# Kernel optimization log

Hardware: AMD Instinct MI355X
Metric: run time of the kernel (lower is better)

## Reference

```python
import jax, jax.numpy as jnp
import numpy as np
from jax import lax

RATE = 2
KSIZE = 3
STRIDE = 1
FUSE_K = 3
SCALE = 10.0
DN = ('NCHW', 'OIHW', 'NCHW')


def extract_patches(x, k, s):
    # x: [B,C,H,W] -> [B,nH,nW,C,k,k]  (ZeroPad2d(1) when k != 1, as in torch code)
    B, C, H, W = x.shape
    p = 0 if k == 1 else 1
    xp = jnp.pad(x, ((0, 0), (0, 0), (p, p), (p, p)))
    nH = (H + 2 * p - k) // s + 1
    nW = (W + 2 * p - k) // s + 1
    cols = [xp[:, :, di:di + s * nH:s, dj:dj + s * nW:s]
            for di in range(k) for dj in range(k)]
    pat = jnp.stack(cols, 0).reshape(k, k, B, C, nH, nW)
    return pat.transpose(2, 4, 5, 3, 0, 1)


def _fuse(y):
    # conv of the [L,L] score image with eye(FUSE_K) kernel, same padding
    # == sum of diagonal shifts of the zero-padded image
    L = y.shape[0]
    p = (FUSE_K - 1) // 2
    A = jnp.pad(y, ((p, p), (p, p)))
    out = A[0:L, 0:L]
    for d in range(1, FUSE_K):
        out = out + A[d:d + L, d:d + L]
    return out


def _per_sample(xi, wi, raw_wi, mmi, h, w):
    # xi: [C,h,w]  wi: [L,C,3,3]  raw_wi: [L,C,4,4]  mmi: [L,1,1]
    L = h * w
    norm = jnp.sqrt(jnp.sum(wi * wi, axis=(1, 2, 3), keepdims=True))
    wi_n = wi / jnp.maximum(norm, 1e-4)
    # cosine-similarity conv: [L,h,w]
    yi = lax.conv_general_dilated(xi[None], wi_n, (1, 1), ((1, 1), (1, 1)),
                                  dimension_numbers=DN)[0]
    # fuse pass 1 on [L(patch), L(spatial)]
    y = _fuse(yi.reshape(L, L))
    # transpose (h_p,w_p,h',w') -> (w_p,h_p,w',h'), fuse pass 2, transpose back
    y = y.reshape(h, w, h, w).transpose(1, 0, 3, 2).reshape(L, L)
    y = _fuse(y)
    y = y.reshape(w, h, w, h).transpose(1, 0, 3, 2).reshape(L, h, w)
    y = y * mmi
    y = jax.nn.softmax(y * SCALE, axis=0)
    y = jnp.maximum(y * mmi, 1e-8)
    # conv_transpose2d(y, raw_wi, stride=2, padding=1) as lhs-dilated conv
    Wf = raw_wi[:, :, ::-1, ::-1].transpose(1, 0, 2, 3)  # [C,L,4,4]
    out = lax.conv_general_dilated(y[None], Wf, (1, 1), ((2, 2), (2, 2)),
                                   lhs_dilation=(2, 2),
                                   dimension_numbers=DN)[0]
    return out / 4.0


def reference(x1, x2, mask):
    B, C, H, W = x1.shape
    kernel = 2 * RATE
    raw_w = extract_patches(x1, kernel, RATE * STRIDE)
    x2s = x2[:, :, ::2, ::2]          # F.interpolate scale=0.5, nearest
    h, w = x2s.shape[2], x2s.shape[3]
    L = h * w
    raw_w = raw_w.reshape(B, L, C, kernel, kernel)
    wpat = extract_patches(x2s, KSIZE, STRIDE).reshape(B, L, C, KSIZE, KSIZE)
    # mask is already [B,1,h,w]: bilinear align_corners resize to (h,w) is identity
    m = extract_patches(mask, KSIZE, STRIDE).reshape(B, L, -1).mean(axis=2)
    mm = (m == 0.0).astype(x1.dtype)[:, :, None, None]  # [B,L,1,1]
    f = lambda xi, wi, rwi, mmi: _per_sample(xi, wi, rwi, mmi, h, w)
    return jax.vmap(f)(x2s, wpat, raw_w, mm)  # [B,C,H,W]


def setup_inputs() -> dict:
    key = jax.random.key(0)
    k1, k2 = jax.random.split(key)
    x1 = jax.random.normal(k1, (2, 128, 96, 96), dtype=jnp.float32)
    x2 = jax.random.normal(k2, (2, 128, 96, 96), dtype=jnp.float32)
    mask = jnp.zeros((2, 1, 48, 48), dtype=jnp.float32)
    return {"x1": x1, "x2": x2, "mask": mask}
```

## Files before the change

kernel.cpp:

```cpp
#include <hip/hip_runtime.h>
#include <hip/hip_bf16.h>

#define Cc   128
#define Hh   96
#define hs   48
#define Ls   2304
#define CK   2048
#define KG   384

typedef __attribute__((ext_vector_type(8))) short short8;
typedef __attribute__((ext_vector_type(4))) float f32x4;

__device__ __forceinline__ unsigned short f2bf(float x) {
    unsigned int u = __float_as_uint(x);
    unsigned int r = (u + 0x7fff + ((u >> 16) & 1)) >> 16;
    return (unsigned short)r;
}
__device__ __forceinline__ float bf2f(unsigned short h) {
    return __uint_as_float((unsigned)h << 16);
}

__device__ __forceinline__ f32x4 ld4u(const float* p) {
    f32x4 v; __builtin_memcpy(&v, p, 16); return v;
}

#define GLOAD_LDS16(g, l) \
    __builtin_amdgcn_global_load_lds((__attribute__((address_space(1))) const void*)(g), \
                                     (__attribute__((address_space(3))) void*)(l), 16, 0, 0)


__global__ __launch_bounds__(256) void transposePQ_k(const float* __restrict__ x2,
                                                     unsigned short* __restrict__ P,
                                                     unsigned short* __restrict__ Q,
                                                     long long sPQ, int z0) {
    const int z = z0 + blockIdx.z;
    const float* x2b = x2 + (size_t)z * Cc * Hh * Hh;
    unsigned short* Pb = P + (size_t)blockIdx.z * sPQ;
    unsigned short* Qb = Q + (size_t)blockIdx.z * sPQ;
    __shared__ float tile[64][65];
    const int c0 = blockIdx.x * 64;
    const int l0 = blockIdx.y * 64;
    const int t = threadIdx.x;
    const int lt = t & 63, cg = t >> 6;
    const int l = l0 + lt;
    const int iy = l / hs, jx = l % hs;
    const int srcoff = iy * (2 * Hh) + 2 * jx;
#pragma unroll
    for (int cc = 0; cc < 16; ++cc) {
        int c = cg * 16 + cc;
        tile[lt][c] = x2b[(size_t)(c0 + c) * (Hh * Hh) + srcoff];
    }
    __syncthreads();
    const int lr = t >> 2, seg = t & 3;
    const int lw = l0 + lr;
    short8 hv0, hv1, lv0, lv1;
#pragma unroll
    for (int k = 0; k < 8; ++k) {
        float x = tile[lr][seg * 16 + k];
        unsigned short h = f2bf(x);
        float hf = __uint_as_float((unsigned)h << 16);
        unsigned short lo = f2bf(x - hf);
        hv0[k] = (short)h; lv0[k] = (short)lo;
    }
#pragma unroll
    for (int k = 0; k < 8; ++k) {
        float x = tile[lr][seg * 16 + 8 + k];
        unsigned short h = f2bf(x);
        float hf = __uint_as_float((unsigned)h << 16);
        unsigned short lo = f2bf(x - hf);
        hv1[k] = (short)h; lv1[k] = (short)lo;
    }
    size_t rowp = (size_t)lw * KG;
    int coff = c0 + seg * 16;
    *(short8*)&Pb[rowp + coff] = hv0;        *(short8*)&Pb[rowp + coff + 8] = hv1;
    *(short8*)&Pb[rowp + 128 + coff] = lv0;  *(short8*)&Pb[rowp + 128 + coff + 8] = lv1;
    *(short8*)&Pb[rowp + 256 + coff] = hv0;  *(short8*)&Pb[rowp + 256 + coff + 8] = hv1;
    *(short8*)&Qb[rowp + coff] = hv0;        *(short8*)&Qb[rowp + coff + 8] = hv1;
    *(short8*)&Qb[rowp + 128 + coff] = hv0;  *(short8*)&Qb[rowp + 128 + coff + 8] = hv1;
    *(short8*)&Qb[rowp + 256 + coff] = lv0;  *(short8*)&Qb[rowp + 256 + coff + 8] = lv1;
}

__global__ __launch_bounds__(256) void mm_k(const float* __restrict__ mask, float* __restrict__ MM) {
    int z = blockIdx.y;
    const float* mb = mask + (size_t)z * hs * hs;
    float* MMb = MM + (size_t)z * Ls;
    int l = blockIdx.x * 256 + threadIdx.x;
    if (l >= Ls) return;
    int ly = l / hs, lx = l % hs;
    float s = 0.f;
    for (int dy = -1; dy <= 1; ++dy)
        for (int dx = -1; dx <= 1; ++dx) {
            int yy = ly + dy, xx = lx + dx;
            if ((unsigned)yy < (unsigned)hs && (unsigned)xx < (unsigned)hs) s += mb[yy * hs + xx];
        }
    float m = s * (1.0f / 9.0f);
    MMb[l] = (m == 0.0f) ? 1.0f : 0.0f;
}

__global__ __launch_bounds__(256) void taps9rn_k(const float* __restrict__ G, float* __restrict__ S,
                                                 float* __restrict__ RN, long long zsG, long long zsS, int z0) {
    const float* Gb = G + (size_t)blockIdx.z * zsG;
    float* Sb = S + (size_t)blockIdx.z * zsS;
    float* RNb = RN + (size_t)(z0 + blockIdx.z) * Ls;
    int g = blockIdx.x * 256 + threadIdx.x;
    int i = g / 576;
    int jb = (g - i * 576) * 4;
    int iy = i / hs, ix = i % hs;
    int jy = jb / hs, jx0 = jb % hs;
    f32x4 acc = {};
#pragma unroll
    for (int dy = -1; dy <= 1; ++dy) {
        int vy = ((unsigned)(iy + dy) < (unsigned)hs) && ((unsigned)(jy + dy) < (unsigned)hs);
#pragma unroll
        for (int dx = -1; dx <= 1; ++dx) {
            int vi = vy && ((unsigned)(ix + dx) < (unsigned)hs);
            int o = hs * dy + dx;
            int row = vi ? (i + o) : i;
            f32x4 v = ld4u(&Gb[(size_t)row * Ls + jb + o]);
            f32x4 m;
#pragma unroll
            for (int ln = 0; ln < 4; ++ln)
                m[ln] = (vi && ((unsigned)(jx0 + ln + dx) < (unsigned)hs)) ? 1.f : 0.f;
            acc += v * m;
        }
    }
    __builtin_memcpy(&Sb[(size_t)i * Ls + jb], &acc, 16);
    int dd = i - jb;
    if ((unsigned)dd < 4u) RNb[i] = 1.0f / fmaxf(sqrtf(acc[dd]), 1e-4f);
}

__global__ __launch_bounds__(256) void fuse12T_k(const float* __restrict__ S, const float* __restrict__ RN,
                                                 float* __restrict__ ZT, long long zsS, long long zsZT, int z0) {
    const float* Sb = S + (size_t)blockIdx.z * zsS;
    float* ZTb = ZT + (size_t)blockIdx.z * zsZT;
    const float* RNb = RN + (size_t)(z0 + blockIdx.z) * Ls;
    __shared__ float tile[64][65];
    const int i0 = blockIdx.y * 64, j0 = blockIdx.x * 64;
    const int t = threadIdx.x;
    const int jg = t & 15, tit = t >> 4;
    const int jb = j0 + jg * 4;
    const int jy0 = jb / hs, jx0 = jb % hs;

    int ccb[9]; f32x4 m4[9];
#pragma unroll
    for (int d2 = -1; d2 <= 1; ++d2) {
        int cl[4], vb[4];
#pragma unroll
        for (int ln = 0; ln < 4; ++ln) {
            int j2 = (jx0 + ln) * hs + jy0 + d2;
            int vv = ((unsigned)j2 < (unsigned)Ls) ? 1 : 0;
            int c = vv ? ((j2 % hs) * hs + j2 / hs) : 0;
            cl[ln] = c; vb[ln] = vv;
        }
        int base = 0;
#pragma unroll
        for (int ln = 0; ln < 4; ++ln) if (vb[ln]) base = cl[ln] - ln;
#pragma unroll
        for (int d1 = -1; d1 <= 1; ++d1) {
            int idx = (d2 + 1) * 3 + (d1 + 1);
            ccb[idx] = base + d1;
            f32x4 mm;
#pragma unroll
            for (int ln = 0; ln < 4; ++ln) {
                int cc = cl[ln] + d1;
                mm[ln] = (vb[ln] && ((unsigned)cc < (unsigned)Ls)) ? 1.f : 0.f;
            }
            m4[idx] = mm;
        }
    }

    f32x4 acc[4] = {};
#pragma unroll
    for (int kk = 0; kk < 4; ++kk) {
        const int i = i0 + tit * 4 + kk;
        const int iy = i / hs, ix = i % hs;
        const int tif = ix * hs + iy;
#pragma unroll
        for (int d2 = -1; d2 <= 1; ++d2) {
            int i2 = tif + d2;
            int vi = ((unsigned)i2 < (unsigned)Ls) ? 1 : 0;
            int r = vi ? ((i2 % hs) * hs + i2 / hs) : 1;
#pragma unroll
            for (int d1 = -1; d1 <= 1; ++d1) {
                int rr = r + d1;
                int vr = vi && ((unsigned)rr < (unsigned)Ls);
                int rrc = vr ? rr : 0;
                float w = RNb[rrc];
                w = vr ? w : 0.f;
                int idx = (d2 + 1) * 3 + (d1 + 1);
                f32x4 v = ld4u(&Sb[(size_t)rrc * Ls + ccb[idx]]);
                acc[kk] += v * m4[idx] * w;
            }
        }
    }
#pragma unroll
    for (int kk = 0; kk < 4; ++kk) {
        int ti = tit * 4 + kk;
        tile[ti][jg * 4 + 0] = acc[kk][0];
        tile[ti][jg * 4 + 1] = acc[kk][1];
        tile[ti][jg * 4 + 2] = acc[kk][2];
        tile[ti][jg * 4 + 3] = acc[kk][3];
    }
    __syncthreads();
    const int r2 = t >> 2, cs = (t & 3) * 16;
    float vbuf[16];
#pragma unroll
    for (int k = 0; k < 16; ++k) vbuf[k] = tile[cs + k][r2];
    float* dst = &ZTb[(size_t)(j0 + r2) * Ls + i0 + cs];
#pragma unroll
    for (int k = 0; k < 4; ++k)
        *(float4*)&dst[k * 4] = *(float4*)&vbuf[k * 4];
}

__global__ __launch_bounds__(256) void softmax_row_k(const float* __restrict__ ZT, const float* __restrict__ MM,
                                                     unsigned short* __restrict__ AT, long long zsZT, int z0) {
    const int z = z0 + blockIdx.z;
    const float* ZTb = ZT + (size_t)blockIdx.z * zsZT;
    const float* MMb = MM + (size_t)z * Ls;
    unsigned short* ATb = AT + (size_t)z * Ls * Ls;
    const int w = threadIdx.x >> 6, lane = threadIdx.x & 63;
    const int p = blockIdx.x * 4 + w;
    const float* row = ZTb + (size_t)p * Ls;
    float v[36];
    float mx = -3.4e38f;
#pragma unroll
    for (int k = 0; k < 9; ++k) {
        const float4 zv = *(const float4*)&row[k * 256 + lane * 4];
        const float4 m = *(const float4*)&MMb[k * 256 + lane * 4];
        v[4 * k + 0] = zv.x * m.x * 10.f;
        v[4 * k + 1] = zv.y * m.y * 10.f;
        v[4 * k + 2] = zv.z * m.z * 10.f;
        v[4 * k + 3] = zv.w * m.w * 10.f;
        mx = fmaxf(mx, fmaxf(fmaxf(v[4 * k], v[4 * k + 1]), fmaxf(v[4 * k + 2], v[4 * k + 3])));
    }
#pragma unroll
    for (int off = 32; off; off >>= 1) mx = fmaxf(mx, __shfl_xor(mx, off));
    float sum = 0.f;
#pragma unroll
    for (int kk = 0; kk < 36; ++kk) { v[kk] = expf(v[kk] - mx); sum += v[kk]; }
#pragma unroll
    for (int off = 32; off; off >>= 1) sum += __shfl_xor(sum, off);
    const float rs = 1.0f / sum;
#pragma unroll
    for (int k = 0; k < 9; ++k) {
        const float4 m = *(const float4*)&MMb[k * 256 + lane * 4];
        ushort4 o;
        o.x = f2bf(fmaxf(v[4 * k + 0] * rs * m.x, 1e-8f));
        o.y = f2bf(fmaxf(v[4 * k + 1] * rs * m.y, 1e-8f));
        o.z = f2bf(fmaxf(v[4 * k + 2] * rs * m.z, 1e-8f));
        o.w = f2bf(fmaxf(v[4 * k + 3] * rs * m.w, 1e-8f));
        *(ushort4*)&ATb[(size_t)p * Ls + k * 256 + lane * 4] = o;
    }
}

__global__ __launch_bounds__(256) void gather_rwT_k(const float* __restrict__ x1, unsigned short* __restrict__ RWT) {
    const int z = blockIdx.z;
    const float* x1b = x1 + (size_t)z * Cc * Hh * Hh;
    unsigned short* R = RWT + (size_t)z * CK * Ls;
    int l = blockIdx.x * 256 + threadIdx.x;
    int ck = blockIdx.y;
    int c = ck >> 4, a = (ck >> 2) & 3, b2 = ck & 3;
    int ly = l / hs, lx = l % hs;
    int u = 2 * ly + a - 1, vv = 2 * lx + b2 - 1;
    float val = ((unsigned)u < (unsigned)Hh && (unsigned)vv < (unsigned)Hh) ? x1b[c * (Hh * Hh) + u * Hh + vv] : 0.0f;
    R[(size_t)ck * Ls + l] = f2bf(val);
}

__global__ __launch_bounds__(256) void scatter3_k(const unsigned short* __restrict__ T, float* __restrict__ out) {
    const int z = blockIdx.z;
    const int c = blockIdx.x;
    const int yh = blockIdx.y;
    const unsigned short* Tb = T + (size_t)z * Ls * CK + (size_t)c * 16;
    float* outb = out + (size_t)z * Cc * Hh * Hh + (size_t)c * Hh * Hh;
    const int i0 = (yh == 0) ? 0 : 23;
    __shared__ unsigned short Tl[1200 * 16];
    const int t = threadIdx.x;
#pragma unroll
    for (int rep = 0; rep < 5; ++rep) {
        int p = rep * 256 + t;
        if (p < 1200)
            __builtin_memcpy(&Tl[p * 16], &Tb[(size_t)(i0 * hs + p) * CK], 32);
    }
    __syncthreads();
#pragma unroll
    for (int rep = 0; rep < 5; ++rep) {
        int idx4 = rep * 256 + t;
        if (idx4 >= 1152) break;
        int Y = yh * 48 + idx4 / 24;
        int X0 = (idx4 % 24) * 4;
        float o4[4];
#pragma unroll
        for (int xi = 0; xi < 4; ++xi) {
            int X = X0 + xi;
            int a0 = (Y + 1) & 1, b0 = (X + 1) & 1;
            float s = 0.f;
#pragma unroll
            for (int ai = 0; ai < 2; ++ai) {
                int a = a0 + 2 * ai;
                int i = (Y + 1 - a) >> 1;
                if ((unsigned)i >= (unsigned)hs) continue;
#pragma unroll
                for (int bi = 0; bi < 2; ++bi) {
                    int b2 = b0 + 2 * bi;
                    int jj = (X + 1 - b2) >> 1;
                    if ((unsigned)jj >= (unsigned)hs) continue;
                    s += bf2f(Tl[((i - i0) * hs + jj) * 16 + a * 4 + b2]);
                }
            }
            o4[xi] = 0.25f * s;
        }
        *(float4*)&outb[Y * Hh + X0] = *(float4*)&o4[0];
    }
}

template <int SUPER, int CBF16>
__global__ __launch_bounds__(256) void mfma_gemm_k(const unsigned short* __restrict__ A,
                                                   const unsigned short* __restrict__ Bt,
                                                   void* __restrict__ Cv, int M, int N, int K,
                                                   long long sA, long long sB, long long sC) {
    A  += (size_t)blockIdx.z * sA;
    Bt += (size_t)blockIdx.z * sB;
    float* Cf = (float*)Cv + (CBF16 ? 0 : (size_t)blockIdx.z * sC);
    unsigned short* Ch = (unsigned short*)Cv + (CBF16 ? (size_t)blockIdx.z * sC : 0);

    const int nb = gridDim.x * gridDim.y;
    const int flat = blockIdx.y * gridDim.x + blockIdx.x;
    const int q = nb >> 3, r = nb & 7;
    const int xcd = flat & 7, sidx = flat >> 3;
    const int wg = (xcd < r ? xcd * (q + 1) : r * (q + 1) + (xcd - r) * q) + sidx;
    int bm, bn;
    if (SUPER) {
        int st = wg / 12, tt = wg % 12;
        int stn = st & 3, stm = st >> 2;
        int tn = tt & 3, tm = tt >> 2;
        bn = (stn * 4 + tn) * 128;
        bm = (stm * 3 + tm) * 128;
    } else {
        bm = (wg / gridDim.x) * 128;
        bn = (wg % gridDim.x) * 128;
    }

    __shared__ __align__(16) unsigned short Asm[2][128 * 32];
    __shared__ __align__(16) unsigned short Bsm[2][128 * 32];
    const int t = threadIdx.x;
    const int lane = t & 63, w = t >> 6;
    const int wr = w >> 1, wc = w & 1;

    const int rA = 32 * w + (lane >> 2);
    const int kA = (((lane & 3) ^ ((lane >> 3) & 3))) * 8;
    const unsigned short* gA0 = A + (size_t)(bm + rA) * K + kA;
    const unsigned short* gA1 = gA0 + (size_t)16 * K;
    const unsigned short* gB0 = Bt + (size_t)(bn + rA) * K + kA;
    const unsigned short* gB1 = gB0 + (size_t)16 * K;

#define STAGE4(b, koff) do { \
        GLOAD_LDS16(gA0 + (koff), &Asm[b][(2 * w) * 512]); \
        GLOAD_LDS16(gA1 + (koff), &Asm[b][(2 * w + 1) * 512]); \
        GLOAD_LDS16(gB0 + (koff), &Bsm[b][(2 * w) * 512]); \
        GLOAD_LDS16(gB1 + (koff), &Bsm[b][(2 * w + 1) * 512]); \
    } while (0)

    const int fr = lane & 15, fq = lane >> 4;
    const int sxa = (fr >> 1) & 3;
    const int sqa = (fq ^ sxa) * 8;
    f32x4 acc[4][4] = {};

    const int nt = K >> 5;
    STAGE4(0, 0);
    __syncthreads();
    int cur = 0;
    for (int tt = 0; tt < nt; ++tt) {
        if (tt + 1 < nt) STAGE4(cur ^ 1, (tt + 1) * 32);
        short8 av[4], bv[4];
#pragma unroll
        for (int m = 0; m < 4; ++m)
            av[m] = *(const short8*)&Asm[cur][(wr * 64 + m * 16 + fr) * 32 + sqa];
#pragma unroll
        for (int n = 0; n < 4; ++n)
            bv[n] = *(const short8*)&Bsm[cur][(wc * 64 + n * 16 + fr) * 32 + sqa];
#pragma unroll
        for (int m = 0; m < 4; ++m)
#pragma unroll
            for (int n = 0; n < 4; ++n)
                acc[m][n] = __builtin_amdgcn_mfma_f32_16x16x32_bf16(av[m], bv[n], acc[m][n], 0, 0, 0);
        __syncthreads();
        cur ^= 1;
    }
#undef STAGE4

#pragma unroll
    for (int m = 0; m < 4; ++m) {
        int row0 = bm + wr * 64 + m * 16 + fq * 4;
#pragma unroll
        for (int n = 0; n < 4; ++n) {
            int col = bn + wc * 64 + n * 16 + fr;
#pragma unroll
            for (int rr = 0; rr < 4; ++rr) {
                if (CBF16)
                    Ch[(size_t)(row0 + rr) * N + col] = f2bf(acc[m][n][rr]);
                else
                    Cf[(size_t)(row0 + rr) * N + col] = acc[m][n][rr];
            }
        }
    }
}


extern "C" void kernel_launch(void* const* d_in, const int* in_sizes, int n_in,
                              void* d_out, int out_size, void* d_ws, size_t ws_size,
                              hipStream_t stream) {
    const float* x1 = (const float*)d_in[0];
    const float* x2 = (const float*)d_in[1];
    const float* mask = (const float*)d_in[2];
    float* out = (float*)d_out;

    char* base = (char*)d_ws;
    const size_t LsLs = (size_t)Ls * Ls;
    const size_t LsCK = (size_t)Ls * CK;
    const long long sPQ = (long long)Ls * KG;

    const bool batched = ws_size >= 132175872ull;

    float* MM2 = (float*)(base);
    float* RN2 = (float*)(base + 20480);
    unsigned short *P, *Q, *ATb2, *RWT2;
    float *G, *S;
    unsigned short* T2 = (unsigned short*)base;
    if (batched) {
        P    = (unsigned short*)(base + 40960);
        Q    = (unsigned short*)(base + 3584000);
        G    = (float*)(base + 7127040);
        S    = (float*)(base + 49598464);
        ATb2 = (unsigned short*)(base + 92067840);
        RWT2 = (unsigned short*)(base + 113301504);
    } else {
        P    = (unsigned short*)(base + 40960);
        Q    = (unsigned short*)(base + 1812480);
        G    = (float*)(base + 3586048);
        S    = (float*)(base + 24823808);
        ATb2 = (unsigned short*)(base + 46059520);
        RWT2 = (unsigned short*)(base + 67293184);
    }

    mm_k<<<dim3(Ls / 256, 2), 256, 0, stream>>>(mask, MM2);
    gather_rwT_k<<<dim3(Ls / 256, CK, 2), 256, 0, stream>>>(x1, RWT2);

    const int tapsGrid = (Ls * 576) / 256;

    if (batched) {
        transposePQ_k<<<dim3(2, Ls / 64, 2), 256, 0, stream>>>(x2, P, Q, sPQ, 0);
        mfma_gemm_k<0, 0><<<dim3(Ls / 128, Ls / 128, 2), 256, 0, stream>>>(
            P, Q, G, Ls, Ls, KG, sPQ, sPQ, (long long)LsLs);
        taps9rn_k<<<dim3(tapsGrid, 1, 2), 256, 0, stream>>>(G, S, RN2, (long long)LsLs, (long long)LsLs, 0);
        fuse12T_k<<<dim3(Ls / 64, Ls / 64, 2), 256, 0, stream>>>(S, RN2, G, (long long)LsLs, (long long)LsLs, 0);
        softmax_row_k<<<dim3(Ls / 4, 1, 2), 256, 0, stream>>>(G, MM2, ATb2, (long long)LsLs, 0);
    } else {
        for (int z0 = 0; z0 < 2; ++z0) {
            transposePQ_k<<<dim3(2, Ls / 64, 1), 256, 0, stream>>>(x2, P, Q, 0, z0);
            mfma_gemm_k<0, 0><<<dim3(Ls / 128, Ls / 128, 1), 256, 0, stream>>>(
                P, Q, G, Ls, Ls, KG, 0, 0, 0);
            taps9rn_k<<<dim3(tapsGrid, 1, 1), 256, 0, stream>>>(G, S, RN2, 0, 0, z0);
            fuse12T_k<<<dim3(Ls / 64, Ls / 64, 1), 256, 0, stream>>>(S, RN2, G, 0, 0, z0);
            softmax_row_k<<<dim3(Ls / 4, 1, 1), 256, 0, stream>>>(G, MM2, ATb2, 0, z0);
        }
    }

    mfma_gemm_k<1, 1><<<dim3(CK / 128, Ls / 128, 2), 256, 0, stream>>>(
        ATb2, RWT2, T2, Ls, CK, Ls,
        (long long)LsLs, (long long)LsCK, (long long)LsCK);

    scatter3_k<<<dim3(Cc, 2, 2), 256, 0, stream>>>(T2, out);

    (void)in_sizes; (void)n_in; (void)out_size; (void)ws_size;
}
```

Baseline: 222.1 us.

## Use 8-wave GEMM blocks and vectorize the raw-patch gather kernel

The MFMA GEMM moves from 4 waves to 8 waves per 128x128 tile. Each wave now computes a 32x64 sub-tile and stages one 16-row slice of A and B per k-step, which halves the accumulator registers per wave and doubles the waves available to hide latency. Separately, the raw-weight gather kernel now has each thread produce 8 consecutive bf16 outputs and write them as one 16-byte store, replacing one scalar store per thread across a huge grid. The trade-off is that twice as many waves synchronise on the same LDS buffers, and each wave issues fewer MFMAs per LDS read.

```diff
diff --git a/kernel.cpp b/kernel.cpp
--- a/kernel.cpp
+++ b/kernel.cpp
@@ -257,13 +257,24 @@
     const int z = blockIdx.z;
     const float* x1b = x1 + (size_t)z * Cc * Hh * Hh;
     unsigned short* R = RWT + (size_t)z * CK * Ls;
-    int l = blockIdx.x * 256 + threadIdx.x;
-    int ck = blockIdx.y;
+    int idx = blockIdx.x * 256 + threadIdx.x;
+    int ck = idx / 288;
+    int lg = idx - ck * 288;
+    int l0 = lg * 8;
+    int ly = lg / 6;
+    int lx0 = (lg - ly * 6) * 8;
     int c = ck >> 4, a = (ck >> 2) & 3, b2 = ck & 3;
-    int ly = l / hs, lx = l % hs;
-    int u = 2 * ly + a - 1, vv = 2 * lx + b2 - 1;
-    float val = ((unsigned)u < (unsigned)Hh && (unsigned)vv < (unsigned)Hh) ? x1b[c * (Hh * Hh) + u * Hh + vv] : 0.0f;
-    R[(size_t)ck * Ls + l] = f2bf(val);
+    int u = 2 * ly + a - 1;
+    short8 o = {};
+    if ((unsigned)u < (unsigned)Hh) {
+        const float* row = x1b + (size_t)c * (Hh * Hh) + (size_t)u * Hh;
+#pragma unroll
+        for (int e = 0; e < 8; ++e) {
+            int vv = 2 * (lx0 + e) + b2 - 1;
+            o[e] = (short)(((unsigned)vv < (unsigned)Hh) ? f2bf(row[vv]) : (unsigned short)0);
+        }
+    }
+    *(short8*)&R[(size_t)ck * Ls + l0] = o;
 }
 
 __global__ __launch_bounds__(256) void scatter3_k(const unsigned short* __restrict__ T, float* __restrict__ out) {
@@ -314,7 +325,7 @@
 }
 
 template <int SUPER, int CBF16>
-__global__ __launch_bounds__(256) void mfma_gemm_k(const unsigned short* __restrict__ A,
+__global__ __launch_bounds__(512) void mfma_gemm_k(const unsigned short* __restrict__ A,
                                                    const unsigned short* __restrict__ Bt,
                                                    void* __restrict__ Cv, int M, int N, int K,
                                                    long long sA, long long sB, long long sC) {
@@ -346,51 +357,46 @@
     const int lane = t & 63, w = t >> 6;
     const int wr = w >> 1, wc = w & 1;
 
-    const int rA = 32 * w + (lane >> 2);
-    const int kA = (((lane & 3) ^ ((lane >> 3) & 3))) * 8;
-    const unsigned short* gA0 = A + (size_t)(bm + rA) * K + kA;
-    const unsigned short* gA1 = gA0 + (size_t)16 * K;
-    const unsigned short* gB0 = Bt + (size_t)(bn + rA) * K + kA;
-    const unsigned short* gB1 = gB0 + (size_t)16 * K;
-
-#define STAGE4(b, koff) do { \
-        GLOAD_LDS16(gA0 + (koff), &Asm[b][(2 * w) * 512]); \
-        GLOAD_LDS16(gA1 + (koff), &Asm[b][(2 * w + 1) * 512]); \
-        GLOAD_LDS16(gB0 + (koff), &Bsm[b][(2 * w) * 512]); \
-        GLOAD_LDS16(gB1 + (koff), &Bsm[b][(2 * w + 1) * 512]); \
+    const int rA = 16 * w + (lane >> 2);
+    const int kA = ((lane & 3) ^ ((lane >> 3) & 3)) * 8;
+    const unsigned short* gA = A + (size_t)(bm + rA) * K + kA;
+    const unsigned short* gB = Bt + (size_t)(bn + rA) * K + kA;
+
+#define STAGE2(b, koff) do { \
+        GLOAD_LDS16(gA + (koff), &Asm[b][w * 512]); \
+        GLOAD_LDS16(gB + (koff), &Bsm[b][w * 512]); \
     } while (0)
 
     const int fr = lane & 15, fq = lane >> 4;
-    const int sxa = (fr >> 1) & 3;
-    const int sqa = (fq ^ sxa) * 8;
-    f32x4 acc[4][4] = {};
+    const int sqa = (fq ^ ((fr >> 1) & 3)) * 8;
+    f32x4 acc[2][4] = {};
 
     const int nt = K >> 5;
-    STAGE4(0, 0);
+    STAGE2(0, 0);
     __syncthreads();
     int cur = 0;
     for (int tt = 0; tt < nt; ++tt) {
-        if (tt + 1 < nt) STAGE4(cur ^ 1, (tt + 1) * 32);
-        short8 av[4], bv[4];
-#pragma unroll
-        for (int m = 0; m < 4; ++m)
-            av[m] = *(const short8*)&Asm[cur][(wr * 64 + m * 16 + fr) * 32 + sqa];
+        if (tt + 1 < nt) STAGE2(cur ^ 1, (tt + 1) * 32);
+        short8 av[2], bv[4];
+#pragma unroll
+        for (int m = 0; m < 2; ++m)
+            av[m] = *(const short8*)&Asm[cur][(wr * 32 + m * 16 + fr) * 32 + sqa];
 #pragma unroll
         for (int n = 0; n < 4; ++n)
             bv[n] = *(const short8*)&Bsm[cur][(wc * 64 + n * 16 + fr) * 32 + sqa];
 #pragma unroll
-        for (int m = 0; m < 4; ++m)
+        for (int m = 0; m < 2; ++m)
 #pragma unroll
             for (int n = 0; n < 4; ++n)
                 acc[m][n] = __builtin_amdgcn_mfma_f32_16x16x32_bf16(av[m], bv[n], acc[m][n], 0, 0, 0);
         __syncthreads();
         cur ^= 1;
     }
-#undef STAGE4
-
-#pragma unroll
-    for (int m = 0; m < 4; ++m) {
-        int row0 = bm + wr * 64 + m * 16 + fq * 4;
+#undef STAGE2
+
+#pragma unroll
+    for (int m = 0; m < 2; ++m) {
+        int row0 = bm + wr * 32 + m * 16 + fq * 4;
 #pragma unroll
         for (int n = 0; n < 4; ++n) {
             int col = bn + wc * 64 + n * 16 + fr;
@@ -443,13 +449,13 @@
     }
 
     mm_k<<<dim3(Ls / 256, 2), 256, 0, stream>>>(mask, MM2);
-    gather_rwT_k<<<dim3(Ls / 256, CK, 2), 256, 0, stream>>>(x1, RWT2);
+    gather_rwT_k<<<dim3((CK * 288) / 256, 1, 2), 256, 0, stream>>>(x1, RWT2);
 
     const int tapsGrid = (Ls * 576) / 256;
 
     if (batched) {
         transposePQ_k<<<dim3(2, Ls / 64, 2), 256, 0, stream>>>(x2, P, Q, sPQ, 0);
-        mfma_gemm_k<0, 0><<<dim3(Ls / 128, Ls / 128, 2), 256, 0, stream>>>(
+        mfma_gemm_k<0, 0><<<dim3(Ls / 128, Ls / 128, 2), 512, 0, stream>>>(
             P, Q, G, Ls, Ls, KG, sPQ, sPQ, (long long)LsLs);
         taps9rn_k<<<dim3(tapsGrid, 1, 2), 256, 0, stream>>>(G, S, RN2, (long long)LsLs, (long long)LsLs, 0);
         fuse12T_k<<<dim3(Ls / 64, Ls / 64, 2), 256, 0, stream>>>(S, RN2, G, (long long)LsLs, (long long)LsLs, 0);
@@ -457,7 +463,7 @@
     } else {
         for (int z0 = 0; z0 < 2; ++z0) {
             transposePQ_k<<<dim3(2, Ls / 64, 1), 256, 0, stream>>>(x2, P, Q, 0, z0);
-            mfma_gemm_k<0, 0><<<dim3(Ls / 128, Ls / 128, 1), 256, 0, stream>>>(
+            mfma_gemm_k<0, 0><<<dim3(Ls / 128, Ls / 128, 1), 512, 0, stream>>>(
                 P, Q, G, Ls, Ls, KG, 0, 0, 0);
             taps9rn_k<<<dim3(tapsGrid, 1, 1), 256, 0, stream>>>(G, S, RN2, 0, 0, z0);
             fuse12T_k<<<dim3(Ls / 64, Ls / 64, 1), 256, 0, stream>>>(S, RN2, G, 0, 0, z0);
@@ -465,7 +471,7 @@
         }
     }
 
-    mfma_gemm_k<1, 1><<<dim3(CK / 128, Ls / 128, 2), 256, 0, stream>>>(
+    mfma_gemm_k<1, 1><<<dim3(CK / 128, Ls / 128, 2), 512, 0, stream>>>(
         ATb2, RWT2, T2, Ls, CK, Ls,
         (long long)LsLs, (long long)LsCK, (long long)LsCK);
 
```

After: 230.4 us. 1.04x slower.
